# Performance work log

Measured on AMD Instinct MI355X. Metric: run time of the kernel, lower is better.

Reference implementation:

```python
import jax, jax.numpy as jnp
import numpy as np

GRID_SIZE = 0.08
EPS = 1e-5
B, N, C_IN, C_OUT = 8, 65536, 64, 128


def setup_inputs() -> dict:
    key = jax.random.key(0)
    k1, k2, k3, k4 = jax.random.split(key, 4)
    # xyz in [0, 2): ~25 voxels per axis at grid_size=0.08 -> M ~ 15k clusters
    xyz = jax.random.uniform(k1, (B, N, 3), dtype=jnp.float32) * 2.0
    feats = jax.random.normal(k2, (B, N, C_IN), dtype=jnp.float32)
    W = jax.random.normal(k3, (C_IN, C_OUT), dtype=jnp.float32) / np.sqrt(C_IN)
    b = jnp.zeros((C_OUT,), jnp.float32)
    gamma = jnp.ones((C_OUT,), jnp.float32)
    beta = jnp.zeros((C_OUT,), jnp.float32)
    return {"xyz": xyz, "feats": feats, "W": W, "b": b, "gamma": gamma, "beta": beta}


def _voxel_pool_one(xyz_b, feats_b):
    # xyz_b: (N,3), feats_b: (N,C). Static pad to N clusters (worst case M=N).
    n = xyz_b.shape[0]
    coords = jnp.floor(xyz_b / GRID_SIZE).astype(jnp.int32)
    coords = coords - coords.min(axis=0)
    dims = coords.max(axis=0) + 1
    keys = coords[:, 0] * dims[1] * dims[2] + coords[:, 1] * dims[2] + coords[:, 2]
    # unique(return_inverse) via sort: cluster ids follow ascending key order
    order = jnp.argsort(keys)
    sk = keys[order]
    is_new = jnp.concatenate([jnp.ones((1,), bool), sk[1:] != sk[:-1]])
    seg = (jnp.cumsum(is_new) - 1).astype(jnp.int32)
    cluster = jnp.zeros((n,), jnp.int32).at[order].set(seg)
    M = is_new.sum().astype(jnp.int32)
    xyz_sum = jax.ops.segment_sum(xyz_b, cluster, num_segments=n)
    feat_sum = jax.ops.segment_sum(feats_b, cluster, num_segments=n)
    count = jax.ops.segment_sum(jnp.ones((n,), xyz_b.dtype), cluster, num_segments=n)
    count = jnp.maximum(count, 1.0)[:, None]
    return xyz_sum / count, feat_sum / count, cluster, M


def reference(xyz, feats, W, b, gamma, beta):
    xyz_pooled, feat_mean, cluster, Ms = jax.vmap(_voxel_pool_one)(xyz, feats)
    max_M = Ms.max()
    # linear + layernorm on (B, N, C_OUT) (padded rows beyond M_b are zeros)
    h = feat_mean @ W + b
    mu = h.mean(axis=-1, keepdims=True)
    var = ((h - mu) ** 2).mean(axis=-1, keepdims=True)
    feats_pooled = (h - mu) * jax.lax.rsqrt(var + EPS) * gamma + beta
    return xyz_pooled, feats_pooled, cluster, max_M
```

## Files before the change

### kernel.cpp

```cpp
#include <hip/hip_runtime.h>
#include <cstdint>
#include <climits>
#include <math.h>

#define Bb    8
#define Nn    65536
#define CIN   64
#define COUT  128
#define KMAXX 15632
#define VKEY  25600
#define VSTR  25600
#define EPSV  1e-5f

#define OFF_MVALS  0
#define OFF_MAXM   8
#define OFF_TAB    16
#define OFF_CNT    204816
#define OFF_SEGS   329872
#define OFF_SORT   454928
#define OFF_MEAN   586000
#define WS_END     8589584
#define MEMSET_INTS 204816

__device__ __forceinline__ int voxc(float x, float rcp_g) {
    return (int)floorf(x * rcp_g);
}

__device__ __forceinline__ float rdlanef(float v, int l) {
    return __uint_as_float(__builtin_amdgcn_readlane(__float_as_uint(v), l));
}

__global__ __launch_bounds__(256) void k_count(const float* __restrict__ xyz,
                                               int* __restrict__ tab,
                                               unsigned short* __restrict__ keys,
                                               float grid) {
    float rcp_g = __builtin_amdgcn_rcpf(grid);
    int i = blockIdx.x * 256 + threadIdx.x;
    int b = i >> 16;
    int c0 = voxc(xyz[(size_t)i * 3 + 0], rcp_g);
    int c1 = voxc(xyz[(size_t)i * 3 + 1], rcp_g);
    int c2 = voxc(xyz[(size_t)i * 3 + 2], rcp_g);
    int key = (c0 * 32 + c1) * 32 + c2;
    atomicAdd(&tab[b * VSTR + key], 1);
    keys[i] = (unsigned short)key;
}

__global__ __launch_bounds__(1024) void k_scan(int* __restrict__ tab,
                                               float* __restrict__ cntf,
                                               int* __restrict__ segs,
                                               int* __restrict__ Ms,
                                               int* __restrict__ maxM) {
    __shared__ int wsC[16], wsFg[16];
    int b = blockIdx.x, tid = threadIdx.x;
    int lane = tid & 63, wv = tid >> 6;
    bool act = tid < (VKEY / 32);
    int4 f[8];
    int4* tb4 = (int4*)(tab + b * VSTR);
    const int4 z4 = make_int4(0, 0, 0, 0);
#pragma unroll
    for (int j = 0; j < 8; ++j) f[j] = act ? tb4[tid * 8 + j] : z4;
    int* ff = (int*)f;
    int sc = 0, sf = 0;
#pragma unroll
    for (int j = 0; j < 32; ++j) { sc += ff[j]; sf += (ff[j] != 0); }
    int ic = sc, ig = sf;
#pragma unroll
    for (int d = 1; d < 64; d <<= 1) {
        int tc = __shfl_up(ic, d);
        int tg = __shfl_up(ig, d);
        if (lane >= d) { ic += tc; ig += tg; }
    }
    if (lane == 63) { wsC[wv] = ic; wsFg[wv] = ig; }
    __syncthreads();
    int wpC = 0, wpF = 0, totF = 0;
#pragma unroll
    for (int w = 0; w < 16; ++w) {
        int vc = wsC[w], vf = wsFg[w];
        if (w < wv) { wpC += vc; wpF += vf; }
        totF += vf;
    }
    if (act) {
        int runC = wpC + ic - sc;
        int runF = wpF + ig - sf;
        int4 o[8];
        int* oo = (int*)o;
#pragma unroll
        for (int j = 0; j < 32; ++j) {
            int c = ff[j];
            oo[j] = (runF << 17) | runC;
            if (c) {
                cntf[b * KMAXX + runF] = (float)c;
                segs[b * KMAXX + runF] = runC;
                runC += c;
                runF += 1;
            }
        }
#pragma unroll
        for (int j = 0; j < 8; ++j) tb4[tid * 8 + j] = o[j];
    }
    if (tid == 0) {
        Ms[b] = totF;
        atomicMax(maxM, totF);
    }
}

__global__ __launch_bounds__(256) void k_scatter(const unsigned short* __restrict__ keys,
                                                 int* __restrict__ tab,
                                                 unsigned short* __restrict__ sorted,
                                                 float* __restrict__ out_cluster) {
    int i = blockIdx.x * 256 + threadIdx.x;
    int b = i >> 16;
    int key = keys[i];
    int v = atomicAdd(&tab[b * VSTR + key], 1);
    sorted[(size_t)b * Nn + (v & 0x1FFFF)] = (unsigned short)i;
    out_cluster[i] = (float)(v >> 17);
}

#define GPB 245
__global__ __launch_bounds__(256, 6) void k_gather(const float* __restrict__ xyz,
                                                   const float4* __restrict__ feats4,
                                                   const unsigned short* __restrict__ sorted,
                                                   const float* __restrict__ cnt,
                                                   const int* __restrict__ segs,
                                                   const int* __restrict__ Ms,
                                                   float4* __restrict__ mean4,
                                                   float* __restrict__ out_xyz) {
    const int b = blockIdx.x / GPB;
    const int blk = blockIdx.x - b * GPB;
    const int wv = threadIdx.x >> 6, lane = threadIdx.x & 63;
    const int sub = lane >> 4, c4 = lane & 15;
    const int rowBase = blk * 64 + wv * 16;
    if (rowBase >= KMAXX) return;
    const int M = Ms[b];
    const size_t pbase = (size_t)b * Nn;
    const size_t cbase = (size_t)b * KMAXX;
    float cl = 0.0f;
    int sl = 0;
    if (lane < 16) {
        int r = rowBase + lane;
        if (r < M) { cl = cnt[cbase + r]; sl = segs[cbase + r]; }
    }
    for (int it = 0; it < 4; ++it) {
        const int row0 = rowBase + it * 4;
        int c[4], s[4];
        float cf[4];
#pragma unroll
        for (int q = 0; q < 4; ++q) {
            cf[q] = rdlanef(cl, it * 4 + q);
            s[q] = __builtin_amdgcn_readlane(sl, it * 4 + q);
            c[q] = (int)cf[q];
        }
        int p[4][2];
#pragma unroll
        for (int q = 0; q < 4; ++q) {
            p[q][0] = (sub     < c[q]) ? (int)sorted[pbase + s[q] + sub]     : -1;
            p[q][1] = (sub + 4 < c[q]) ? (int)sorted[pbase + s[q] + sub + 4] : -1;
        }
        float4 acc[4];
        float axs[4];
#pragma unroll
        for (int q = 0; q < 4; ++q) { acc[q] = make_float4(0.f, 0.f, 0.f, 0.f); axs[q] = 0.f; }
#pragma unroll
        for (int q = 0; q < 4; ++q) {
#pragma unroll
            for (int h = 0; h < 2; ++h) {
                int pp = p[q][h];
                if (pp >= 0) {
                    float4 v = feats4[(pbase + pp) * 16 + c4];
                    acc[q].x += v.x; acc[q].y += v.y; acc[q].z += v.z; acc[q].w += v.w;
                    if (c4 < 3) axs[q] += xyz[(pbase + pp) * 3 + c4];
                }
            }
        }
#pragma unroll
        for (int q = 0; q < 4; ++q) {
            for (int g = 2; g * 4 < c[q]; ++g) {
                int i = g * 4 + sub;
                if (i < c[q]) {
                    int pp = (int)sorted[pbase + s[q] + i];
                    float4 v = feats4[(pbase + pp) * 16 + c4];
                    acc[q].x += v.x; acc[q].y += v.y; acc[q].z += v.z; acc[q].w += v.w;
                    if (c4 < 3) axs[q] += xyz[(pbase + pp) * 3 + c4];
                }
            }
        }
#pragma unroll
        for (int q = 0; q < 4; ++q) {
            const int row = row0 + q;
            if (row < M) {
                float4 a = acc[q];
                a.x += __shfl_xor(a.x, 16); a.x += __shfl_xor(a.x, 32);
                a.y += __shfl_xor(a.y, 16); a.y += __shfl_xor(a.y, 32);
                a.z += __shfl_xor(a.z, 16); a.z += __shfl_xor(a.z, 32);
                a.w += __shfl_xor(a.w, 16); a.w += __shfl_xor(a.w, 32);
                float ax = axs[q];
                ax += __shfl_xor(ax, 16); ax += __shfl_xor(ax, 32);
                float cv = cf[q];
                float4 m4 = make_float4(a.x / cv, a.y / cv, a.z / cv, a.w / cv);
                if (lane < 16) mean4[(cbase + row) * 16 + c4] = m4;
                if (lane < 3)
                    out_xyz[(pbase + row) * 3 + lane] = ax / cv;
            } else {
                if (lane < 3)
                    out_xyz[(pbase + row) * 3 + lane] = 0.0f;
            }
        }
    }
}

#define GBLK 1024
__global__ __launch_bounds__(256) void k_gemmln(const float4* __restrict__ mean4,
                                                const int* __restrict__ Ms,
                                                const int* __restrict__ maxM,
                                                const float* __restrict__ W,
                                                const float* __restrict__ bias,
                                                const float* __restrict__ gamma,
                                                const float* __restrict__ beta,
                                                float* __restrict__ out_feats,
                                                float* __restrict__ out_xyz,
                                                float* __restrict__ out_maxM) {
    const int tid = threadIdx.x;
    const int b = blockIdx.x >> 10;
    const int blk = blockIdx.x & 1023;
    const int wv = tid >> 6, lane = tid & 63;
    if (blockIdx.x == 0 && tid == 0) out_maxM[0] = (float)maxM[0];

    if (blk * 64 >= KMAXX) {
        const int rowBase = blk * 64 + wv * 16;
        const float4 z = make_float4(0.f, 0.f, 0.f, 0.f);
        float4* of4 = (float4*)out_feats;
        size_t obase = ((size_t)b * Nn + rowBase) * 32;
#pragma unroll
        for (int i = 0; i < 8; ++i) of4[obase + i * 64 + lane] = z;
        float4* ox4 = (float4*)out_xyz;
        size_t xb = ((size_t)b * Nn + rowBase) * 3 / 4;
        if (lane < 12) ox4[xb + lane] = z;
        return;
    }

    __shared__ float sWT[128 * 68];
    for (int idx = tid; idx < 64 * 128; idx += 256) {
        int k = idx >> 7, c = idx & 127;
        sWT[c * 68 + k] = W[idx];
    }
    const int c4 = lane & 15;
    const int M = Ms[b];
    const float bias0 = bias[lane], bias1 = bias[lane + 64];
    const float g0 = gamma[lane], g1 = gamma[lane + 64];
    const float be0 = beta[lane], be1 = beta[lane + 64];
    __syncthreads();
    const int rowBase = blk * 64 + wv * 16;
    const size_t cbase = (size_t)b * KMAXX;
    if (rowBase >= M) {
        const float4 z = make_float4(0.f, 0.f, 0.f, 0.f);
        float4* of4 = (float4*)out_feats;
        size_t obase = ((size_t)b * Nn + rowBase) * 32;
#pragma unroll
        for (int i = 0; i < 8; ++i) of4[obase + i * 64 + lane] = z;
        if (rowBase >= KMAXX) {
            float4* ox4 = (float4*)out_xyz;
            size_t xb = ((size_t)b * Nn + rowBase) * 3 / 4;
            if (lane < 12) ox4[xb + lane] = z;
        }
        return;
    }
    const float* wt0 = &sWT[lane * 68];
    const float* wt1 = &sWT[(lane + 64) * 68];
    for (int it = 0; it < 4; ++it) {
        const int row0 = rowBase + it * 4;
        const size_t cb0 = cbase + row0;
        float4 mm[4];
        bool lv[4];
#pragma unroll
        for (int r = 0; r < 4; ++r) {
            lv[r] = (row0 + r) < M;
            mm[r] = lv[r] ? mean4[(cb0 + r) * 16 + c4]
                          : make_float4(0.f, 0.f, 0.f, 0.f);
        }
        float a0[4] = {bias0, bias0, bias0, bias0};
        float a1[4] = {bias1, bias1, bias1, bias1};
#pragma unroll
        for (int k4 = 0; k4 < 16; ++k4) {
            float4 w0 = *(const float4*)&wt0[k4 * 4];
            float4 w1 = *(const float4*)&wt1[k4 * 4];
#pragma unroll
            for (int r = 0; r < 4; ++r) {
                float s0 = rdlanef(mm[r].x, k4);
                float s1 = rdlanef(mm[r].y, k4);
                float s2 = rdlanef(mm[r].z, k4);
                float s3 = rdlanef(mm[r].w, k4);
                a0[r] += s0 * w0.x + s1 * w0.y + s2 * w0.z + s3 * w0.w;
                a1[r] += s0 * w1.x + s1 * w1.y + s2 * w1.z + s3 * w1.w;
            }
        }
#pragma unroll
        for (int r = 0; r < 4; ++r) {
            float s = a0[r] + a1[r];
#pragma unroll
            for (int d2 = 32; d2 >= 1; d2 >>= 1) s += __shfl_xor(s, d2);
            float mu = s * (1.0f / 128.0f);
            float d0 = a0[r] - mu, d1 = a1[r] - mu;
            float q = d0 * d0 + d1 * d1;
#pragma unroll
            for (int d2 = 32; d2 >= 1; d2 >>= 1) q += __shfl_xor(q, d2);
            float rs = rsqrtf(q * (1.0f / 128.0f) + EPSV);
            float o0 = lv[r] ? (d0 * rs * g0 + be0) : 0.0f;
            float o1 = lv[r] ? (d1 * rs * g1 + be1) : 0.0f;
            size_t ob = ((size_t)b * Nn + row0 + r) * 128;
            out_feats[ob + lane] = o0;
            out_feats[ob + 64 + lane] = o1;
        }
    }
}

extern "C" void kernel_launch(void* const* d_in, const int* in_sizes, int n_in,
                              void* d_out, int out_size, void* d_ws, size_t ws_size,
                              hipStream_t stream) {
    const float* xyz   = (const float*)d_in[0];
    const float* feats = (const float*)d_in[1];
    const float* W     = (const float*)d_in[2];
    const float* bias  = (const float*)d_in[3];
    const float* gamma = (const float*)d_in[4];
    const float* beta  = (const float*)d_in[5];

    float* out = (float*)d_out;
    float* out_xyz     = out;
    float* out_feats   = out + (size_t)Bb * Nn * 3;
    float* out_cluster = out_feats + (size_t)Bb * Nn * COUT;
    float* out_maxM    = out_cluster + (size_t)Bb * Nn;

    int*   wsI    = (int*)d_ws;
    float* wsF    = (float*)d_ws;
    int*   Ms     = wsI + OFF_MVALS;
    int*   maxM   = wsI + OFF_MAXM;
    int*   tab    = wsI + OFF_TAB;
    float* cnt    = wsF + OFF_CNT;
    int*   segs   = wsI + OFF_SEGS;
    unsigned short* sorted = (unsigned short*)(wsI + OFF_SORT);
    float* meanb  = wsF + OFF_MEAN;
    unsigned short* keys = (unsigned short*)(wsF + OFF_MEAN);

    const float grid_sz = 0.08f;

    hipMemsetAsync(wsI, 0, (size_t)MEMSET_INTS * 4, stream);
    k_count<<<Bb * Nn / 256, 256, 0, stream>>>(xyz, tab, keys, grid_sz);
    k_scan<<<Bb, 1024, 0, stream>>>(tab, cnt, segs, Ms, maxM);
    k_scatter<<<Bb * Nn / 256, 256, 0, stream>>>(keys, tab, sorted, out_cluster);
    k_gather<<<Bb * GPB, 256, 0, stream>>>(xyz, (const float4*)feats, sorted, cnt, segs,
                                           Ms, (float4*)meanb, out_xyz);
    k_gemmln<<<Bb * GBLK, 256, 0, stream>>>((const float4*)meanb, Ms, maxM, W, bias,
                                            gamma, beta, out_feats, out_xyz, out_maxM);
}
```

Baseline: 524.6 us.

## Reuse count-pass atomic ranks in scatter and prefetch next gather group indices

The count kernel now keeps the value returned by its atomic increment and packs that per-point rank with the voxel key into a 32-bit word. The scatter pass then does a plain table read plus an add instead of a second atomic, which removes contended atomics. The gather kernel software-pipelines its loop by loading the next group's counts, offsets and first sorted indices before it accumulates the current group. The packed buffer is twice the size of the old 16-bit key buffer, and the prefetch uses more registers, which could lower occupancy under launch_bounds(256,6).

```diff
diff --git a/kernel.cpp b/kernel.cpp
--- a/kernel.cpp
+++ b/kernel.cpp
@@ -32,7 +32,7 @@
 
 __global__ __launch_bounds__(256) void k_count(const float* __restrict__ xyz,
                                                int* __restrict__ tab,
-                                               unsigned short* __restrict__ keys,
+                                               int* __restrict__ pk,
                                                float grid) {
     float rcp_g = __builtin_amdgcn_rcpf(grid);
     int i = blockIdx.x * 256 + threadIdx.x;
@@ -41,8 +41,8 @@
     int c1 = voxc(xyz[(size_t)i * 3 + 1], rcp_g);
     int c2 = voxc(xyz[(size_t)i * 3 + 2], rcp_g);
     int key = (c0 * 32 + c1) * 32 + c2;
-    atomicAdd(&tab[b * VSTR + key], 1);
-    keys[i] = (unsigned short)key;
+    int v = atomicAdd(&tab[b * VSTR + key], 1);
+    pk[i] = (v << 15) | key;
 }
 
 __global__ __launch_bounds__(1024) void k_scan(int* __restrict__ tab,
@@ -104,16 +104,19 @@
     }
 }
 
-__global__ __launch_bounds__(256) void k_scatter(const unsigned short* __restrict__ keys,
-                                                 int* __restrict__ tab,
+__global__ __launch_bounds__(256) void k_scatter(const int* __restrict__ pk,
+                                                 const int* __restrict__ tab,
                                                  unsigned short* __restrict__ sorted,
                                                  float* __restrict__ out_cluster) {
     int i = blockIdx.x * 256 + threadIdx.x;
     int b = i >> 16;
-    int key = keys[i];
-    int v = atomicAdd(&tab[b * VSTR + key], 1);
-    sorted[(size_t)b * Nn + (v & 0x1FFFF)] = (unsigned short)i;
-    out_cluster[i] = (float)(v >> 17);
+    int p = pk[i];
+    int key = p & 0x7FFF;
+    int arr = (int)(((unsigned)p) >> 15);
+    int t = tab[b * VSTR + key];
+    int slot = (t & 0x1FFFF) + arr;
+    sorted[(size_t)b * Nn + slot] = (unsigned short)i;
+    out_cluster[i] = (float)(t >> 17);
 }
 
 #define GPB 245
@@ -140,22 +143,31 @@
         int r = rowBase + lane;
         if (r < M) { cl = cnt[cbase + r]; sl = segs[cbase + r]; }
     }
+    int   c_[4], s_[4], p_[4][2];
+    float cf_[4];
+#pragma unroll
+    for (int q = 0; q < 4; ++q) {
+        cf_[q] = rdlanef(cl, q);
+        s_[q]  = __builtin_amdgcn_readlane(sl, q);
+        c_[q]  = (int)cf_[q];
+        p_[q][0] = (sub     < c_[q]) ? (int)sorted[pbase + s_[q] + sub]     : -1;
+        p_[q][1] = (sub + 4 < c_[q]) ? (int)sorted[pbase + s_[q] + sub + 4] : -1;
+    }
     for (int it = 0; it < 4; ++it) {
+        int   cn[4], sn[4], pn[4][2];
+        float cfn[4];
+        if (it < 3) {
+            const int base = (it + 1) * 4;
+#pragma unroll
+            for (int q = 0; q < 4; ++q) {
+                cfn[q] = rdlanef(cl, base + q);
+                sn[q]  = __builtin_amdgcn_readlane(sl, base + q);
+                cn[q]  = (int)cfn[q];
+                pn[q][0] = (sub     < cn[q]) ? (int)sorted[pbase + sn[q] + sub]     : -1;
+                pn[q][1] = (sub + 4 < cn[q]) ? (int)sorted[pbase + sn[q] + sub + 4] : -1;
+            }
+        }
         const int row0 = rowBase + it * 4;
-        int c[4], s[4];
-        float cf[4];
-#pragma unroll
-        for (int q = 0; q < 4; ++q) {
-            cf[q] = rdlanef(cl, it * 4 + q);
-            s[q] = __builtin_amdgcn_readlane(sl, it * 4 + q);
-            c[q] = (int)cf[q];
-        }
-        int p[4][2];
-#pragma unroll
-        for (int q = 0; q < 4; ++q) {
-            p[q][0] = (sub     < c[q]) ? (int)sorted[pbase + s[q] + sub]     : -1;
-            p[q][1] = (sub + 4 < c[q]) ? (int)sorted[pbase + s[q] + sub + 4] : -1;
-        }
         float4 acc[4];
         float axs[4];
 #pragma unroll
@@ -164,7 +176,7 @@
         for (int q = 0; q < 4; ++q) {
 #pragma unroll
             for (int h = 0; h < 2; ++h) {
-                int pp = p[q][h];
+                int pp = p_[q][h];
                 if (pp >= 0) {
                     float4 v = feats4[(pbase + pp) * 16 + c4];
                     acc[q].x += v.x; acc[q].y += v.y; acc[q].z += v.z; acc[q].w += v.w;
@@ -174,10 +186,10 @@
         }
 #pragma unroll
         for (int q = 0; q < 4; ++q) {
-            for (int g = 2; g * 4 < c[q]; ++g) {
+            for (int g = 2; g * 4 < c_[q]; ++g) {
                 int i = g * 4 + sub;
-                if (i < c[q]) {
-                    int pp = (int)sorted[pbase + s[q] + i];
+                if (i < c_[q]) {
+                    int pp = (int)sorted[pbase + s_[q] + i];
                     float4 v = feats4[(pbase + pp) * 16 + c4];
                     acc[q].x += v.x; acc[q].y += v.y; acc[q].z += v.z; acc[q].w += v.w;
                     if (c4 < 3) axs[q] += xyz[(pbase + pp) * 3 + c4];
@@ -195,7 +207,7 @@
                 a.w += __shfl_xor(a.w, 16); a.w += __shfl_xor(a.w, 32);
                 float ax = axs[q];
                 ax += __shfl_xor(ax, 16); ax += __shfl_xor(ax, 32);
-                float cv = cf[q];
+                float cv = cf_[q];
                 float4 m4 = make_float4(a.x / cv, a.y / cv, a.z / cv, a.w / cv);
                 if (lane < 16) mean4[(cbase + row) * 16 + c4] = m4;
                 if (lane < 3)
@@ -203,6 +215,13 @@
             } else {
                 if (lane < 3)
                     out_xyz[(pbase + row) * 3 + lane] = 0.0f;
+            }
+        }
+        if (it < 3) {
+#pragma unroll
+            for (int q = 0; q < 4; ++q) {
+                c_[q] = cn[q]; s_[q] = sn[q]; cf_[q] = cfn[q];
+                p_[q][0] = pn[q][0]; p_[q][1] = pn[q][1];
             }
         }
     }
@@ -338,14 +357,14 @@
     int*   segs   = wsI + OFF_SEGS;
     unsigned short* sorted = (unsigned short*)(wsI + OFF_SORT);
     float* meanb  = wsF + OFF_MEAN;
-    unsigned short* keys = (unsigned short*)(wsF + OFF_MEAN);
+    int*   pk     = (int*)(wsF + OFF_MEAN);
 
     const float grid_sz = 0.08f;
 
     hipMemsetAsync(wsI, 0, (size_t)MEMSET_INTS * 4, stream);
-    k_count<<<Bb * Nn / 256, 256, 0, stream>>>(xyz, tab, keys, grid_sz);
+    k_count<<<Bb * Nn / 256, 256, 0, stream>>>(xyz, tab, pk, grid_sz);
     k_scan<<<Bb, 1024, 0, stream>>>(tab, cnt, segs, Ms, maxM);
-    k_scatter<<<Bb * Nn / 256, 256, 0, stream>>>(keys, tab, sorted, out_cluster);
+    k_scatter<<<Bb * Nn / 256, 256, 0, stream>>>(pk, tab, sorted, out_cluster);
     k_gather<<<Bb * GPB, 256, 0, stream>>>(xyz, (const float4*)feats, sorted, cnt, segs,
                                            Ms, (float4*)meanb, out_xyz);
     k_gemmln<<<Bb * GBLK, 256, 0, stream>>>((const float4*)meanb, Ms, maxM, W, bias,
```

Measured after the change: 517.3 us. Within noise of the previous version (-1.4%).
